# Kernel optimization log

Measured on AMD Instinct MI355X. Metric: run time of the kernel, lower is better.

The kernel has to match this reference:

```python
import jax, jax.numpy as jnp
import numpy as np

LAYERS, HIDDEN, FFN, HEADS = 4, 512, 1024, 4
B, S = 2, 2048
HD = HIDDEN // HEADS  # head size = 128
SCALE_BASE = 512.0
EPS = 1e-5


def _xpos(x, downscale):
    # x: (B, H, S, hd). Faithful to torchscale XPOS with offset=0.
    seq, hd = x.shape[-2], x.shape[-1]
    half = hd // 2
    s = (jnp.arange(0, hd, 2, dtype=jnp.float32) + 0.4 * hd) / (1.4 * hd)  # (half,)
    pos = jnp.arange(seq, dtype=jnp.float32)
    scale = s[None, :] ** (pos[:, None] / SCALE_BASE)  # (S, half)
    inv_freq = 1.0 / (10000.0 ** (jnp.arange(half, dtype=jnp.float32) / half))
    ang = pos[:, None] * inv_freq[None, :]  # (S, half)
    sin, cos = jnp.sin(ang), jnp.cos(ang)
    if downscale:
        scale = 1.0 / scale
    sin_s = jnp.repeat(sin * scale, 2, axis=-1)  # duplicate_interleave -> (S, hd)
    cos_s = jnp.repeat(cos * scale, 2, axis=-1)
    x1, x2 = x[..., ::2], x[..., 1::2]
    rot = jnp.stack([-x2, x1], axis=-1).reshape(x.shape)  # rotate_every_two
    return x * cos_s + rot * sin_s


def _decay_mask(seq, heads):
    gammas = 1.0 - jnp.exp(jnp.linspace(jnp.log(1.0 / 32.0), jnp.log(1.0 / 512.0), heads))
    n = jnp.arange(seq)[:, None]
    m = jnp.arange(seq)[None, :]
    diff = n - m
    pw = gammas[:, None, None] ** jnp.maximum(diff, 0)[None].astype(jnp.float32)
    return jnp.where(diff[None] >= 0, pw, 0.0)  # (H, S, S)


def _ln(x, w, b):
    mu = x.mean(-1, keepdims=True)
    var = x.var(-1, keepdims=True)
    return (x - mu) / jnp.sqrt(var + EPS) * w + b


def _gn(y, w, b, heads):
    # GroupNorm(heads, D) applied on rows of (B*S, D)
    bb, ss, d = y.shape
    hs = d // heads
    yr = y.reshape(bb, ss, heads, hs)
    mu = yr.mean(-1, keepdims=True)
    var = yr.var(-1, keepdims=True)
    yn = ((yr - mu) / jnp.sqrt(var + EPS)).reshape(bb, ss, d)
    return yn * w + b


def setup_inputs() -> dict:
    key = jax.random.key(0)
    ks = jax.random.split(key, 17)
    sc = 1.0 / HIDDEN
    inp = {
        'X': jax.random.normal(ks[0], (B, S, HIDDEN), dtype=jnp.float32),
        'Wq': jax.random.normal(ks[1], (LAYERS, HEADS, HIDDEN, HD), dtype=jnp.float32) * sc,
        'Wk': jax.random.normal(ks[2], (LAYERS, HEADS, HIDDEN, HD), dtype=jnp.float32) * sc,
        'Wv': jax.random.normal(ks[3], (LAYERS, HEADS, HIDDEN, HD), dtype=jnp.float32) * sc,
        'Wg': jax.random.normal(ks[4], (LAYERS, HIDDEN, HIDDEN), dtype=jnp.float32) * sc,
        'Wo': jax.random.normal(ks[5], (LAYERS, HIDDEN, HIDDEN), dtype=jnp.float32) * sc,
        'gn_w': jnp.ones((LAYERS, HIDDEN), dtype=jnp.float32),
        'gn_b': jnp.zeros((LAYERS, HIDDEN), dtype=jnp.float32),
        'ln1_w': jnp.ones((LAYERS, HIDDEN), dtype=jnp.float32),
        'ln1_b': jnp.zeros((LAYERS, HIDDEN), dtype=jnp.float32),
        'ln2_w': jnp.ones((LAYERS, HIDDEN), dtype=jnp.float32),
        'ln2_b': jnp.zeros((LAYERS, HIDDEN), dtype=jnp.float32),
        'f1_w': jax.random.normal(ks[6], (LAYERS, HIDDEN, FFN), dtype=jnp.float32) * (1.0 / np.sqrt(HIDDEN)),
        'f1_b': jnp.zeros((LAYERS, FFN), dtype=jnp.float32),
        'f2_w': jax.random.normal(ks[7], (LAYERS, FFN, HIDDEN), dtype=jnp.float32) * (1.0 / np.sqrt(FFN)),
        'f2_b': jnp.zeros((LAYERS, HIDDEN), dtype=jnp.float32),
    }
    return inp


def reference(X, Wq, Wk, Wv, Wg, Wo, gn_w, gn_b, ln1_w, ln1_b, ln2_w, ln2_b, f1_w, f1_b, f2_w, f2_b):
    bb, ss, d = X.shape
    Dm = _decay_mask(ss, HEADS)  # (H, S, S)
    for i in range(LAYERS):
        Xn = _ln(X, ln1_w[i], ln1_b[i])
        Q = jnp.einsum('bsd,hde->bhse', Xn, Wq[i])
        K = jnp.einsum('bsd,hde->bhse', Xn, Wk[i])
        V = jnp.einsum('bsd,hde->bhse', Xn, Wv[i])
        Q = _xpos(Q, downscale=False)
        K = _xpos(K, downscale=True)
        att = jnp.einsum('bhse,bhte->bhst', Q, K) * Dm[None]
        ret = jnp.einsum('bhst,bhte->bhse', att, V)  # (B,H,S,hd)
        Yh = ret.transpose(0, 2, 1, 3).reshape(bb, ss, d)
        Yg = _gn(Yh, gn_w[i], gn_b[i], HEADS)
        msr = (jax.nn.silu(Xn @ Wg[i]) * Yg) @ Wo[i]
        Y = msr + X
        Yn = _ln(Y, ln2_w[i], ln2_b[i])
        X = jax.nn.gelu(Yn @ f1_w[i] + f1_b[i], approximate=False) @ f2_w[i] + f2_b[i] + Y
    return X
```

## Files before the change

### kernel.cpp

```cpp
#include <hip/hip_runtime.h>
#include <hip/hip_bf16.h>
#include <cstdint>
#include <cstddef>

#define SEQ_ 2048

typedef __bf16 v8bf __attribute__((ext_vector_type(8)));
typedef float v4f __attribute__((ext_vector_type(4)));

__device__ __forceinline__ unsigned short f2bf(float f) {
  unsigned u = __float_as_uint(f);
  return (unsigned short)((u + 0x7FFFu + ((u >> 16) & 1u)) >> 16);
}
__device__ __forceinline__ float bf2f(unsigned short h) {
  return __uint_as_float(((unsigned)h) << 16);
}
__device__ __forceinline__ float silu_(float x) { return x / (1.f + expf(-x)); }
__device__ __forceinline__ float gelu_(float x) { return 0.5f * x * (1.f + erff(x * 0.70710678118654752f)); }

__device__ __forceinline__ void gl_lds16(const void* g, void* l) {
  __builtin_amdgcn_global_load_lds((const __attribute__((address_space(1))) void*)g,
                                   (__attribute__((address_space(3))) void*)l, 16, 0, 0);
}

template <int ROWS>
__device__ __forceinline__ void stage_t(const unsigned short* gsrc, int ldk, char* lds, int tid) {
  const int wid = tid >> 6;
#pragma unroll
  for (int p = 0; p < ROWS / 32; ++p) {
    const int L = p * 256 + tid;
    const int row = L >> 3, slot = L & 7;
    gl_lds16((const char*)(gsrc + (size_t)row * ldk) + ((slot * 16) ^ ((row & 7) << 4)),
             lds + (p * 256 + wid * 64) * 16);
  }
}

__device__ __forceinline__ void stage256(const char* gbase, int srow, char* lds, int tid) {
  const int wid = tid >> 6;
#pragma unroll
  for (int q = 0; q < 8; ++q) {
    const int L = q * 256 + tid;
    const int row = L >> 4;
    const int slot = L & 15;
    gl_lds16(gbase + (size_t)row * srow + ((slot * 16) ^ ((row & 7) << 4)),
             lds + (q * 256 + wid * 64) * 16);
  }
}

__global__ __launch_bounds__(256) void setup_k(const float* __restrict__ Wq, const float* __restrict__ Wk,
                                               const float* __restrict__ Wv, const float* __restrict__ Wg,
                                               const float* __restrict__ Wo, const float* __restrict__ f1w,
                                               const float* __restrict__ f2w, float* __restrict__ tab,
                                               unsigned short* __restrict__ WTQ, unsigned short* __restrict__ WTO,
                                               unsigned short* __restrict__ WF1, unsigned short* __restrict__ WF2) {
  const int b = blockIdx.x, tid = threadIdx.x;
  if (b < 512) {
    const int idx = b * 256 + tid;
    const int pos = idx >> 6, i = idx & 63;
    const float si = (2.f * (float)i + 51.2f) * (1.f / 179.2f);
    const float sc = powf(si, (float)pos * (1.f / 512.f));
    const float invf = powf(10000.f, -(float)i * (1.f / 64.f));
    const float ang = (float)pos * invf;
    const float cs = cosf(ang), sn = sinf(ang);
    tab[idx] = cs * sc;
    tab[131072 + idx] = sn * sc;
    tab[262144 + idx] = cs / sc;
    tab[393216 + idx] = sn / sc;
  } else if (b < 512 + 16384) {
    const size_t idx = (size_t)(b - 512) * 256 + tid;
    const int k = (int)(idx & 511);
    const int n = (int)((idx >> 9) & 2047);
    const int l = (int)(idx >> 20);
    const int sec = n >> 9;
    float v;
    if (sec == 0) {
      const int h = (n >> 7) & 3, e = n & 127;
      v = Wq[(((size_t)l * 4 + h) * 512 + k) * 128 + e];
    } else if (sec == 1) {
      const int h = (n >> 7) & 3, e = n & 127;
      v = Wk[(((size_t)l * 4 + h) * 512 + k) * 128 + e];
    } else if (sec == 2) {
      const int h = (n >> 7) & 3, e = n & 127;
      v = Wv[(((size_t)l * 4 + h) * 512 + k) * 128 + e];
    } else {
      const int c = n & 511;
      v = Wg[((size_t)l * 512 + k) * 512 + c];
    }
    WTQ[idx] = f2bf(v);
  } else if (b < 512 + 16384 + 4096) {
    const size_t idx = (size_t)(b - 512 - 16384) * 256 + tid;
    const int k = (int)(idx & 511);
    const int n = (int)((idx >> 9) & 511);
    const int l = (int)(idx >> 18);
    WTO[idx] = f2bf(Wo[((size_t)l * 512 + k) * 512 + n]);
  } else if (b < 512 + 16384 + 4096 + 8192) {
    const size_t idx = (size_t)(b - 512 - 16384 - 4096) * 256 + tid;
    const int k = (int)(idx & 511);
    const int n = (int)((idx >> 9) & 1023);
    const int l = (int)(idx >> 19);
    WF1[idx] = f2bf(f1w[((size_t)l * 512 + k) * 1024 + n]);
  } else {
    const size_t idx = (size_t)(b - 512 - 16384 - 4096 - 8192) * 256 + tid;
    const int k = (int)(idx & 1023);
    const int n = (int)((idx >> 10) & 511);
    const int l = (int)(idx >> 19);
    WF2[idx] = f2bf(f2w[((size_t)l * 1024 + k) * 512 + n]);
  }
}

__global__ __launch_bounds__(256) void ln_bf_k(const float* __restrict__ x, const float* __restrict__ w,
                                               const float* __restrict__ bv, unsigned short* __restrict__ out) {
  const int row = blockIdx.x * 4 + (threadIdx.x >> 6);
  const int lane = threadIdx.x & 63;
  const float* xr = x + (size_t)row * 512 + lane * 8;
  const float4 v0 = *(const float4*)xr;
  const float4 v1 = *(const float4*)(xr + 4);
  float va[8] = {v0.x, v0.y, v0.z, v0.w, v1.x, v1.y, v1.z, v1.w};
  float s = 0.f, ss = 0.f;
#pragma unroll
  for (int j = 0; j < 8; ++j) { s += va[j]; ss += va[j] * va[j]; }
#pragma unroll
  for (int o = 1; o < 64; o <<= 1) { s += __shfl_xor(s, o); ss += __shfl_xor(ss, o); }
  const float mu = s * (1.f / 512.f);
  const float var = ss * (1.f / 512.f) - mu * mu;
  const float rstd = rsqrtf(var + 1e-5f);
  const int c = lane * 8;
  unsigned short o16[8];
#pragma unroll
  for (int j = 0; j < 8; ++j) o16[j] = f2bf((va[j] - mu) * rstd * w[c + j] + bv[c + j]);
  uint4 pk;
  pk.x = o16[0] | ((unsigned)o16[1] << 16);
  pk.y = o16[2] | ((unsigned)o16[3] << 16);
  pk.z = o16[4] | ((unsigned)o16[5] << 16);
  pk.w = o16[6] | ((unsigned)o16[7] << 16);
  *(uint4*)(out + (size_t)row * 512 + c) = pk;
}

template <int BM, int BN, int EPI>
__global__ __launch_bounds__(256) void mm_k(
    const unsigned short* __restrict__ A, const unsigned short* __restrict__ Bt, const int K,
    const float* __restrict__ t_qc, const float* __restrict__ t_qs,
    const float* __restrict__ t_kc, const float* __restrict__ t_ks,
    unsigned short* __restrict__ o_q, unsigned short* __restrict__ o_k,
    unsigned short* __restrict__ o_ktw, unsigned short* __restrict__ o_vt,
    unsigned short* __restrict__ o_g0,
    const float* __restrict__ auxf, const float* __restrict__ auxf2,
    float* __restrict__ o_f32, unsigned short* __restrict__ o_bf16) {
  constexpr int MR = BM / 32, NR = BN / 32;
  constexpr int BMB = BM * 128, BNB = BN * 128;
  __shared__ __align__(16) char smem[2 * (BMB + BNB)];
  const int tid = threadIdx.x, lane = tid & 63, wid = tid >> 6;
  const int wr = wid >> 1, wc = wid & 1;
  const int l15 = lane & 15, l4 = lane >> 4;
  const int m0 = blockIdx.x * BM, n0 = blockIdx.y * BN;
  const int N = gridDim.y * BN;
  v4f acc[MR][NR];
#pragma unroll
  for (int i = 0; i < MR; ++i)
#pragma unroll
    for (int j = 0; j < NR; ++j) acc[i][j] = v4f{0.f, 0.f, 0.f, 0.f};

  const unsigned short* Ab = A + (size_t)m0 * K;
  const unsigned short* Bb = Bt + (size_t)n0 * K;
  const int NT = K >> 6;
  int cur = 0;
  stage_t<BM>(Ab, K, smem, tid);
  stage_t<BN>(Bb, K, smem + 2 * BMB, tid);
  __syncthreads();
  for (int t = 0; t < NT; ++t) {
    if (t + 1 < NT) {
      stage_t<BM>(Ab + (t + 1) * 64, K, smem + (cur ^ 1) * BMB, tid);
      stage_t<BN>(Bb + (t + 1) * 64, K, smem + 2 * BMB + (cur ^ 1) * BNB, tid);
    }
    const char* Ac = smem + cur * BMB;
    const char* Bc = smem + 2 * BMB + cur * BNB;
#pragma unroll
    for (int ks = 0; ks < 2; ++ks) {
      v8bf af[MR], bfv[NR];
#pragma unroll
      for (int i = 0; i < MR; ++i) {
        const int row = wr * (BM / 2) + i * 16 + l15;
        af[i] = *(const v8bf*)(Ac + row * 128 + ((ks * 64 + l4 * 16) ^ ((row & 7) << 4)));
      }
#pragma unroll
      for (int j = 0; j < NR; ++j) {
        const int row = wc * (BN / 2) + j * 16 + l15;
        bfv[j] = *(const v8bf*)(Bc + row * 128 + ((ks * 64 + l4 * 16) ^ ((row & 7) << 4)));
      }
#pragma unroll
      for (int i = 0; i < MR; ++i)
#pragma unroll
        for (int j = 0; j < NR; ++j)
          acc[i][j] = __builtin_amdgcn_mfma_f32_16x16x32_bf16(af[i], bfv[j], acc[i][j], 0, 0, 0);
    }
    __syncthreads();
    cur ^= 1;
  }

  if constexpr (EPI == 0) {
    const int sec = n0 >> 9;
    const int h = (n0 >> 7) & 3;
    const int srow0 = m0 & (SEQ_ - 1);
    const int bh = ((m0 >> 11) << 2) | h;
    unsigned short* sT = (unsigned short*)smem;
    const float gamma = 1.f - expf(-3.4657359028f - 0.9241962407f * (float)h);
    const float l2g = log2f(gamma);
#pragma unroll
    for (int i = 0; i < MR; ++i) {
#pragma unroll
      for (int r = 0; r < 4; ++r) {
        const int rl = wr * (BM / 2) + i * 16 + l4 * 4 + r;
        const int srow = srow0 + rl;
        const float wk = (sec == 1) ? exp2f(l2g * (float)(127 - (rl & 127))) : 0.f;
#pragma unroll
        for (int j = 0; j < NR; ++j) {
          const int cl = wc * (BN / 2) + j * 16 + l15;
          float v = acc[i][j][r];
          if (sec <= 1) {
            const float p = __shfl_xor(v, 1);
            const float* ct = (sec == 0) ? t_qc : t_kc;
            const float* st = (sec == 0) ? t_qs : t_ks;
            const float c_ = ct[srow * 64 + (cl >> 1)];
            const float s_ = st[srow * 64 + (cl >> 1)];
            const float o = (lane & 1) ? fmaf(v, c_, p * s_) : fmaf(v, c_, -p * s_);
            if (sec == 0) {
              o_q[((size_t)bh * SEQ_ + srow) * 128 + cl] = f2bf(o);
            } else {
              o_k[((size_t)bh * SEQ_ + srow) * 128 + cl] = f2bf(o);
              sT[cl * 136 + rl] = f2bf(o * wk);
            }
          } else if (sec == 2) {
            sT[cl * 136 + rl] = f2bf(v);
          } else {
            o_g0[(size_t)(m0 + rl) * 512 + cl] = f2bf(v);
          }
        }
      }
    }
    if (sec == 1 || sec == 2) {
      __syncthreads();
      unsigned short* dstT = ((sec == 1) ? o_ktw : o_vt) + (size_t)bh * 128 * SEQ_ + srow0;
#pragma unroll
      for (int u = 0; u < 8; ++u) {
        const int idx = u * 256 + tid;
        const int d = idx >> 4, j8 = idx & 15;
        *(v8bf*)(dstT + (size_t)d * SEQ_ + j8 * 8) = *(const v8bf*)(sT + d * 136 + j8 * 8);
      }
    }
  } else {
#pragma unroll
    for (int i = 0; i < MR; ++i) {
#pragma unroll
      for (int r = 0; r < 4; ++r) {
        const int row = m0 + wr * (BM / 2) + i * 16 + l4 * 4 + r;
#pragma unroll
        for (int j = 0; j < NR; ++j) {
          const int col = n0 + wc * (BN / 2) + j * 16 + l15;
          const float v = acc[i][j][r];
          if constexpr (EPI == 1) {
            o_f32[(size_t)row * 512 + col] = v + auxf[(size_t)row * 512 + col];
          } else if constexpr (EPI == 2) {
            o_bf16[(size_t)row * N + col] = f2bf(gelu_(v + auxf[col]));
          } else {
            o_f32[(size_t)row * 512 + col] = v + auxf[col] + auxf2[(size_t)row * 512 + col];
          }
        }
      }
    }
  }
}

__global__ __launch_bounds__(256) void ret1_k(const unsigned short* __restrict__ VT,
                                              const unsigned short* __restrict__ KTw,
                                              float* __restrict__ U) {
  __shared__ __align__(16) char lA[32768];
  __shared__ __align__(16) char lB[32768];
  const int bh = blockIdx.x, c = blockIdx.y;
  const int tid = threadIdx.x, lane = tid & 63, wid = tid >> 6;
  const int wr = wid >> 1, wc = wid & 1;
  const int l15 = lane & 15, l4 = lane >> 4;
  stage256((const char*)(VT + (size_t)bh * 128 * SEQ_ + (size_t)c * 128), SEQ_ * 2, lA, tid);
  stage256((const char*)(KTw + (size_t)bh * 128 * SEQ_ + (size_t)c * 128), SEQ_ * 2, lB, tid);
  __syncthreads();
  v4f acc[4][4];
#pragma unroll
  for (int i = 0; i < 4; ++i)
#pragma unroll
    for (int j = 0; j < 4; ++j) acc[i][j] = v4f{0.f, 0.f, 0.f, 0.f};
#pragma unroll
  for (int ks = 0; ks < 4; ++ks) {
    v8bf af[4], bfv[4];
#pragma unroll
    for (int i = 0; i < 4; ++i) {
      const int ra = wr * 64 + i * 16 + l15;
      af[i] = *(const v8bf*)(lA + ra * 256 + ((ks * 64 + l4 * 16) ^ ((ra & 7) << 4)));
      const int rb = wc * 64 + i * 16 + l15;
      bfv[i] = *(const v8bf*)(lB + rb * 256 + ((ks * 64 + l4 * 16) ^ ((rb & 7) << 4)));
    }
#pragma unroll
    for (int i = 0; i < 4; ++i)
#pragma unroll
      for (int j = 0; j < 4; ++j)
        acc[i][j] = __builtin_amdgcn_mfma_f32_16x16x32_bf16(af[i], bfv[j], acc[i][j], 0, 0, 0);
  }
  float* ub = U + ((size_t)bh * 16 + c) * 16384;
#pragma unroll
  for (int i = 0; i < 4; ++i)
#pragma unroll
    for (int r = 0; r < 4; ++r) {
      const int rd = wr * 64 + i * 16 + l4 * 4 + r;
#pragma unroll
      for (int j = 0; j < 4; ++j) {
        const int ce = wc * 64 + j * 16 + l15;
        ub[rd * 128 + ce] = acc[i][j][r];
      }
    }
}

__global__ __launch_bounds__(256) void ret2_k(const float* __restrict__ U, unsigned short* __restrict__ Sb) {
  const int bh = blockIdx.x;
  const int idx = blockIdx.y * 256 + threadIdx.x;
  const int h = bh & 3;
  const float gamma = 1.f - expf(-3.4657359028f - 0.9241962407f * (float)h);
  const float g128 = exp2f(log2f(gamma) * 128.f);
  float s = 0.f;
#pragma unroll
  for (int c = 0; c < 16; ++c) {
    Sb[((size_t)bh * 16 + c) * 16384 + idx] = f2bf(s);
    s = s * g128 + U[((size_t)bh * 16 + c) * 16384 + idx];
  }
}

__global__ __launch_bounds__(256) void ret3_k(
    const unsigned short* __restrict__ Qb, const unsigned short* __restrict__ Kb,
    const unsigned short* __restrict__ VTb, const unsigned short* __restrict__ Sb,
    const unsigned short* __restrict__ G0b, const float* __restrict__ gnw,
    const float* __restrict__ gnb, unsigned short* __restrict__ Gb) {
  __shared__ __align__(16) char lA[32768];
  __shared__ __align__(16) char lB[32768];
  __shared__ float dpw[132];
  __shared__ float rs[2][128][2];
  const int bh = blockIdx.x, c = blockIdx.y;
  const int h = bh & 3, b = bh >> 2;
  const int tid = threadIdx.x, lane = tid & 63, wid = tid >> 6;
  const int wr = wid >> 1, wc = wid & 1;
  const int l15 = lane & 15, l4 = lane >> 4;
  const float gamma = 1.f - expf(-3.4657359028f - 0.9241962407f * (float)h);
  const float l2g = log2f(gamma);
  stage256((const char*)(Qb + ((size_t)bh * SEQ_ + (size_t)c * 128) * 128), 256, lA, tid);
  stage256((const char*)(Sb + ((size_t)bh * 16 + c) * 16384), 256, lB, tid);
  if (tid < 132) dpw[tid] = exp2f(l2g * (float)tid);
  __syncthreads();

  v4f acc[4][4];
#pragma unroll
  for (int i = 0; i < 4; ++i)
#pragma unroll
    for (int j = 0; j < 4; ++j) acc[i][j] = v4f{0.f, 0.f, 0.f, 0.f};

#pragma unroll
  for (int ks = 0; ks < 4; ++ks) {
    v8bf af[4], bfv[4];
#pragma unroll
    for (int i = 0; i < 4; ++i) {
      const int ra = wr * 64 + i * 16 + l15;
      af[i] = *(const v8bf*)(lA + ra * 256 + ((ks * 64 + l4 * 16) ^ ((ra & 7) << 4)));
      const int rb = wc * 64 + i * 16 + l15;
      bfv[i] = *(const v8bf*)(lB + rb * 256 + ((ks * 64 + l4 * 16) ^ ((rb & 7) << 4)));
    }
#pragma unroll
    for (int i = 0; i < 4; ++i)
#pragma unroll
      for (int j = 0; j < 4; ++j)
        acc[i][j] = __builtin_amdgcn_mfma_f32_16x16x32_bf16(af[i], bfv[j], acc[i][j], 0, 0, 0);
  }
#pragma unroll
  for (int i = 0; i < 4; ++i)
#pragma unroll
    for (int r = 0; r < 4; ++r) {
      const float sc = dpw[wr * 64 + i * 16 + l4 * 4 + r + 1];
#pragma unroll
      for (int j = 0; j < 4; ++j) acc[i][j][r] *= sc;
    }
  __syncthreads();
  stage256((const char*)(Kb + ((size_t)bh * SEQ_ + (size_t)c * 128) * 128), 256, lB, tid);
  __syncthreads();

  v4f sacc[4][4];
#pragma unroll
  for (int i = 0; i < 4; ++i)
#pragma unroll
    for (int j = 0; j < 4; ++j) sacc[i][j] = v4f{0.f, 0.f, 0.f, 0.f};
#pragma unroll
  for (int ks = 0; ks < 4; ++ks) {
    v8bf af[4], bfv[4];
#pragma unroll
    for (int i = 0; i < 4; ++i) {
      const int ra = wr * 64 + i * 16 + l15;
      af[i] = *(const v8bf*)(lA + ra * 256 + ((ks * 64 + l4 * 16) ^ ((ra & 7) << 4)));
      const int rb = wc * 64 + i * 16 + l15;
      bfv[i] = *(const v8bf*)(lB + rb * 256 + ((ks * 64 + l4 * 16) ^ ((rb & 7) << 4)));
    }
#pragma unroll
    for (int i = 0; i < 4; ++i)
#pragma unroll
      for (int j = 0; j < 4; ++j)
        sacc[i][j] = __builtin_amdgcn_mfma_f32_16x16x32_bf16(af[i], bfv[j], sacc[i][j], 0, 0, 0);
  }
  __syncthreads();

#pragma unroll
  for (int i = 0; i < 4; ++i)
#pragma unroll
    for (int r = 0; r < 4; ++r) {
      const int jrow = wr * 64 + i * 16 + l4 * 4 + r;
#pragma unroll
      for (int j = 0; j < 4; ++j) {
        const int icol = wc * 64 + j * 16 + l15;
        const int d = jrow - icol;
        const int dc = d < 0 ? 0 : d;
        const float wgt = dpw[dc];
        const float p = (d < 0) ? 0.f : sacc[i][j][r] * wgt;
        *(unsigned short*)(lB + jrow * 256 + ((icol * 2) ^ ((jrow & 7) << 4))) = f2bf(p);
      }
    }
  stage256((const char*)(VTb + (size_t)bh * 128 * SEQ_ + (size_t)c * 128), SEQ_ * 2, lA, tid);
  __syncthreads();

#pragma unroll
  for (int ks = 0; ks < 4; ++ks) {
    v8bf af[4], bfv[4];
#pragma unroll
    for (int i = 0; i < 4; ++i) {
      const int ra = wr * 64 + i * 16 + l15;
      af[i] = *(const v8bf*)(lB + ra * 256 + ((ks * 64 + l4 * 16) ^ ((ra & 7) << 4)));
      const int rb = wc * 64 + i * 16 + l15;
      bfv[i] = *(const v8bf*)(lA + rb * 256 + ((ks * 64 + l4 * 16) ^ ((rb & 7) << 4)));
    }
#pragma unroll
    for (int i = 0; i < 4; ++i)
#pragma unroll
      for (int j = 0; j < 4; ++j)
        acc[i][j] = __builtin_amdgcn_mfma_f32_16x16x32_bf16(af[i], bfv[j], acc[i][j], 0, 0, 0);
  }

#pragma unroll
  for (int i = 0; i < 4; ++i)
#pragma unroll
    for (int r = 0; r < 4; ++r) {
      const int jrow = wr * 64 + i * 16 + l4 * 4 + r;
      float s1 = 0.f, s2 = 0.f;
#pragma unroll
      for (int j = 0; j < 4; ++j) { const float v = acc[i][j][r]; s1 += v; s2 += v * v; }
#pragma unroll
      for (int o = 1; o < 16; o <<= 1) { s1 += __shfl_xor(s1, o); s2 += __shfl_xor(s2, o); }
      if (l15 == 0) { rs[wc][jrow][0] = s1; rs[wc][jrow][1] = s2; }
    }
  __syncthreads();
  const int tbase = b * SEQ_ + c * 128;
#pragma unroll
  for (int i = 0; i < 4; ++i)
#pragma unroll
    for (int r = 0; r < 4; ++r) {
      const int jrow = wr * 64 + i * 16 + l4 * 4 + r;
      const float s1 = rs[0][jrow][0] + rs[1][jrow][0];
      const float s2 = rs[0][jrow][1] + rs[1][jrow][1];
      const float mu = s1 * (1.f / 128.f);
      const float var = s2 * (1.f / 128.f) - mu * mu;
      const float rstd = rsqrtf(var + 1e-5f);
      const size_t t = (size_t)(tbase + jrow);
#pragma unroll
      for (int j = 0; j < 4; ++j) {
        const int dd = wc * 64 + j * 16 + l15;
        const int cc = h * 128 + dd;
        const float g0 = bf2f(G0b[t * 512 + cc]);
        float o = (acc[i][j][r] - mu) * rstd * gnw[cc] + gnb[cc];
        o *= silu_(g0);
        Gb[t * 512 + cc] = f2bf(o);
      }
    }
}

extern "C" void kernel_launch(void* const* d_in, const int* in_sizes, int n_in,
                              void* d_out, int out_size, void* d_ws, size_t ws_size,
                              hipStream_t stream) {
  const float* X = (const float*)d_in[0];
  const float* Wq = (const float*)d_in[1];
  const float* Wk = (const float*)d_in[2];
  const float* Wv = (const float*)d_in[3];
  const float* Wg = (const float*)d_in[4];
  const float* Wo = (const float*)d_in[5];
  const float* gnw = (const float*)d_in[6];
  const float* gnb = (const float*)d_in[7];
  const float* ln1w = (const float*)d_in[8];
  const float* ln1b = (const float*)d_in[9];
  const float* ln2w = (const float*)d_in[10];
  const float* ln2b = (const float*)d_in[11];
  const float* f1w = (const float*)d_in[12];
  const float* f1b = (const float*)d_in[13];
  const float* f2w = (const float*)d_in[14];
  const float* f2b = (const float*)d_in[15];

  char* ws = (char*)d_ws;
  float* TAB = (float*)(ws + 0);
  unsigned short* WTQ = (unsigned short*)(ws + 2097152);
  unsigned short* WTO = (unsigned short*)(ws + 10485760);
  unsigned short* WF1 = (unsigned short*)(ws + 12582912);
  unsigned short* WF2 = (unsigned short*)(ws + 16777216);
  unsigned short* XNb = (unsigned short*)(ws + 20971520);
  unsigned short* Qb  = (unsigned short*)(ws + 25165824);
  unsigned short* Kb  = (unsigned short*)(ws + 29360128);
  unsigned short* KTw = (unsigned short*)(ws + 33554432);
  unsigned short* VTb = (unsigned short*)(ws + 37748736);
  unsigned short* G0b = (unsigned short*)(ws + 46137344);
  unsigned short* Sbf = (unsigned short*)(ws + 50331648);
  unsigned short* Gb  = (unsigned short*)(ws + 54525952);
  float* Y   = (float*)(ws + 58720256);
  float* XB  = (float*)(ws + 67108864);
  unsigned short* F1b = (unsigned short*)(ws + 75497472);
  float* U = (float*)(ws + 75497472);
  float* qc = TAB, * qs = TAB + 131072, * kc = TAB + 262144, * ks = TAB + 393216;

  setup_k<<<37376, 256, 0, stream>>>(Wq, Wk, Wv, Wg, Wo, f1w, f2w, TAB, WTQ, WTO, WF1, WF2);

  const float* Xcur = X;
  for (int l = 0; l < 4; ++l) {
    ln_bf_k<<<1024, 256, 0, stream>>>(Xcur, ln1w + l * 512, ln1b + l * 512, XNb);
    mm_k<128, 128, 0><<<dim3(32, 16), 256, 0, stream>>>(
        XNb, WTQ + (size_t)l * 2048 * 512, 512, qc, qs, kc, ks,
        Qb, Kb, KTw, VTb, G0b, nullptr, nullptr, nullptr, nullptr);
    ret1_k<<<dim3(8, 16), 256, 0, stream>>>(VTb, KTw, U);
    ret2_k<<<dim3(8, 64), 256, 0, stream>>>(U, Sbf);
    ret3_k<<<dim3(8, 16), 256, 0, stream>>>(Qb, Kb, VTb, Sbf, G0b,
                                            gnw + l * 512, gnb + l * 512, Gb);
    mm_k<128, 64, 1><<<dim3(32, 8), 256, 0, stream>>>(
        Gb, WTO + (size_t)l * 512 * 512, 512, nullptr, nullptr, nullptr, nullptr,
        nullptr, nullptr, nullptr, nullptr, nullptr, Xcur, nullptr, Y, nullptr);
    ln_bf_k<<<1024, 256, 0, stream>>>(Y, ln2w + l * 512, ln2b + l * 512, XNb);
    mm_k<128, 128, 2><<<dim3(32, 8), 256, 0, stream>>>(
        XNb, WF1 + (size_t)l * 1024 * 512, 512, nullptr, nullptr, nullptr, nullptr,
        nullptr, nullptr, nullptr, nullptr, nullptr, f1b + l * 1024, nullptr, nullptr, F1b);
    float* outX = (l == 3) ? (float*)d_out : XB;
    mm_k<128, 64, 3><<<dim3(32, 8), 256, 0, stream>>>(
        F1b, WF2 + (size_t)l * 512 * 1024, 1024, nullptr, nullptr, nullptr, nullptr,
        nullptr, nullptr, nullptr, nullptr, nullptr, f2b + l * 512, Y, outX, nullptr);
    Xcur = XB;
  }
}
```

Baseline: 572.7 us.

## Split retention chunk kernel into half-chunks and tile weight transpose via LDS

The retention kernel ret3_k now handles half a 128-row chunk per block, doubling the grid from 128 to 256 blocks. The first half skips the causally-masked upper part of the intra-chunk QK^T and PV products, which cuts wasted MFMA work and raises occupancy on a GPU with many CUs. Separately, the setup kernel transposes and converts the weights in 64x64 tiles through shared memory with vectorized loads and stores, replacing a strided per-element gather. The cost is more code and duplicated Q/S staging across the two half blocks.

```diff
diff --git a/kernel.cpp b/kernel.cpp
--- a/kernel.cpp
+++ b/kernel.cpp
@@ -35,10 +35,11 @@
   }
 }
 
-__device__ __forceinline__ void stage256(const char* gbase, int srow, char* lds, int tid) {
+template <int NROWS>
+__device__ __forceinline__ void stage_rows(const char* gbase, int srow, char* lds, int tid) {
   const int wid = tid >> 6;
 #pragma unroll
-  for (int q = 0; q < 8; ++q) {
+  for (int q = 0; q < NROWS / 16; ++q) {
     const int L = q * 256 + tid;
     const int row = L >> 4;
     const int slot = L & 15;
@@ -66,45 +67,71 @@
     tab[131072 + idx] = sn * sc;
     tab[262144 + idx] = cs / sc;
     tab[393216 + idx] = sn / sc;
-  } else if (b < 512 + 16384) {
-    const size_t idx = (size_t)(b - 512) * 256 + tid;
-    const int k = (int)(idx & 511);
-    const int n = (int)((idx >> 9) & 2047);
-    const int l = (int)(idx >> 20);
-    const int sec = n >> 9;
-    float v;
-    if (sec == 0) {
-      const int h = (n >> 7) & 3, e = n & 127;
-      v = Wq[(((size_t)l * 4 + h) * 512 + k) * 128 + e];
-    } else if (sec == 1) {
-      const int h = (n >> 7) & 3, e = n & 127;
-      v = Wk[(((size_t)l * 4 + h) * 512 + k) * 128 + e];
-    } else if (sec == 2) {
-      const int h = (n >> 7) & 3, e = n & 127;
-      v = Wv[(((size_t)l * 4 + h) * 512 + k) * 128 + e];
-    } else {
-      const int c = n & 511;
-      v = Wg[((size_t)l * 512 + k) * 512 + c];
-    }
-    WTQ[idx] = f2bf(v);
-  } else if (b < 512 + 16384 + 4096) {
-    const size_t idx = (size_t)(b - 512 - 16384) * 256 + tid;
-    const int k = (int)(idx & 511);
-    const int n = (int)((idx >> 9) & 511);
-    const int l = (int)(idx >> 18);
-    WTO[idx] = f2bf(Wo[((size_t)l * 512 + k) * 512 + n]);
-  } else if (b < 512 + 16384 + 4096 + 8192) {
-    const size_t idx = (size_t)(b - 512 - 16384 - 4096) * 256 + tid;
-    const int k = (int)(idx & 511);
-    const int n = (int)((idx >> 9) & 1023);
-    const int l = (int)(idx >> 19);
-    WF1[idx] = f2bf(f1w[((size_t)l * 512 + k) * 1024 + n]);
+    return;
+  }
+  __shared__ float t[64][65];
+  const float* src;
+  unsigned short* dst;
+  int ldn, ldk;
+  int b2 = b - 512;
+  if (b2 < 768) {
+    const int l = b2 / 192, r = b2 % 192, sec = r / 64, r2 = r % 64, h = r2 >> 4, tt = r2 & 15;
+    const int kt = tt >> 1, et = tt & 1;
+    const float* W = (sec == 0) ? Wq : (sec == 1) ? Wk : Wv;
+    src = W + (((size_t)(l * 4 + h) * 512 + kt * 64) * 128 + et * 64);
+    ldn = 128;
+    dst = WTQ + (size_t)l * 1048576 + (size_t)(sec * 512 + h * 128 + et * 64) * 512 + kt * 64;
+    ldk = 512;
+  } else if (b2 < 1024) {
+    b2 -= 768;
+    const int l = b2 >> 6, tt = b2 & 63, kt = tt >> 3, nt = tt & 7;
+    src = Wg + (size_t)l * 262144 + (size_t)kt * 64 * 512 + nt * 64;
+    ldn = 512;
+    dst = WTQ + (size_t)l * 1048576 + (size_t)(1536 + nt * 64) * 512 + kt * 64;
+    ldk = 512;
+  } else if (b2 < 1280) {
+    b2 -= 1024;
+    const int l = b2 >> 6, tt = b2 & 63, kt = tt >> 3, nt = tt & 7;
+    src = Wo + (size_t)l * 262144 + (size_t)kt * 64 * 512 + nt * 64;
+    ldn = 512;
+    dst = WTO + (size_t)l * 262144 + (size_t)nt * 64 * 512 + kt * 64;
+    ldk = 512;
+  } else if (b2 < 1792) {
+    b2 -= 1280;
+    const int l = b2 >> 7, tt = b2 & 127, kt = tt >> 4, nt = tt & 15;
+    src = f1w + (size_t)l * 524288 + (size_t)kt * 64 * 1024 + nt * 64;
+    ldn = 1024;
+    dst = WF1 + (size_t)l * 524288 + (size_t)nt * 64 * 512 + kt * 64;
+    ldk = 512;
   } else {
-    const size_t idx = (size_t)(b - 512 - 16384 - 4096 - 8192) * 256 + tid;
-    const int k = (int)(idx & 1023);
-    const int n = (int)((idx >> 10) & 511);
-    const int l = (int)(idx >> 19);
-    WF2[idx] = f2bf(f2w[((size_t)l * 1024 + k) * 512 + n]);
+    b2 -= 1792;
+    const int l = b2 >> 7, tt = b2 & 127, kt = tt >> 3, nt = tt & 7;
+    src = f2w + (size_t)l * 524288 + (size_t)kt * 64 * 512 + nt * 64;
+    ldn = 512;
+    dst = WF2 + (size_t)l * 524288 + (size_t)nt * 64 * 1024 + kt * 64;
+    ldk = 1024;
+  }
+#pragma unroll
+  for (int p = 0; p < 4; ++p) {
+    const int idx = p * 256 + tid;
+    const int kr = idx >> 4, c4 = (idx & 15) * 4;
+    const float4 v = *(const float4*)(src + (size_t)kr * ldn + c4);
+    t[kr][c4] = v.x; t[kr][c4 + 1] = v.y; t[kr][c4 + 2] = v.z; t[kr][c4 + 3] = v.w;
+  }
+  __syncthreads();
+#pragma unroll
+  for (int p = 0; p < 2; ++p) {
+    const int idx = p * 256 + tid;
+    const int nr = idx >> 3, k8 = (idx & 7) * 8;
+    unsigned short o[8];
+#pragma unroll
+    for (int j = 0; j < 8; ++j) o[j] = f2bf(t[k8 + j][nr]);
+    uint4 pk;
+    pk.x = o[0] | ((unsigned)o[1] << 16);
+    pk.y = o[2] | ((unsigned)o[3] << 16);
+    pk.z = o[4] | ((unsigned)o[5] << 16);
+    pk.w = o[6] | ((unsigned)o[7] << 16);
+    *(uint4*)(dst + (size_t)nr * ldk + k8) = pk;
   }
 }
 
@@ -279,8 +306,8 @@
   const int tid = threadIdx.x, lane = tid & 63, wid = tid >> 6;
   const int wr = wid >> 1, wc = wid & 1;
   const int l15 = lane & 15, l4 = lane >> 4;
-  stage256((const char*)(VT + (size_t)bh * 128 * SEQ_ + (size_t)c * 128), SEQ_ * 2, lA, tid);
-  stage256((const char*)(KTw + (size_t)bh * 128 * SEQ_ + (size_t)c * 128), SEQ_ * 2, lB, tid);
+  stage_rows<128>((const char*)(VT + (size_t)bh * 128 * SEQ_ + (size_t)c * 128), SEQ_ * 2, lA, tid);
+  stage_rows<128>((const char*)(KTw + (size_t)bh * 128 * SEQ_ + (size_t)c * 128), SEQ_ * 2, lB, tid);
   __syncthreads();
   v4f acc[4][4];
 #pragma unroll
@@ -331,144 +358,155 @@
   }
 }
 
-__global__ __launch_bounds__(256) void ret3_k(
-    const unsigned short* __restrict__ Qb, const unsigned short* __restrict__ Kb,
-    const unsigned short* __restrict__ VTb, const unsigned short* __restrict__ Sb,
-    const unsigned short* __restrict__ G0b, const float* __restrict__ gnw,
-    const float* __restrict__ gnb, unsigned short* __restrict__ Gb) {
-  __shared__ __align__(16) char lA[32768];
-  __shared__ __align__(16) char lB[32768];
-  __shared__ float dpw[132];
-  __shared__ float rs[2][128][2];
-  const int bh = blockIdx.x, c = blockIdx.y;
+template <int HF>
+__device__ __forceinline__ void ret3_body(
+    const unsigned short* Qb, const unsigned short* Kb, const unsigned short* VTb,
+    const unsigned short* Sb, const unsigned short* G0b, const float* gnw,
+    const float* gnb, unsigned short* Gb, char* lA, char* lB, const float* dpw,
+    float* rs, int bh, int c, int tid) {
   const int h = bh & 3, b = bh >> 2;
-  const int tid = threadIdx.x, lane = tid & 63, wid = tid >> 6;
+  const int lane = tid & 63, wid = tid >> 6;
   const int wr = wid >> 1, wc = wid & 1;
   const int l15 = lane & 15, l4 = lane >> 4;
-  const float gamma = 1.f - expf(-3.4657359028f - 0.9241962407f * (float)h);
-  const float l2g = log2f(gamma);
-  stage256((const char*)(Qb + ((size_t)bh * SEQ_ + (size_t)c * 128) * 128), 256, lA, tid);
-  stage256((const char*)(Sb + ((size_t)bh * 16 + c) * 16384), 256, lB, tid);
-  if (tid < 132) dpw[tid] = exp2f(l2g * (float)tid);
-  __syncthreads();
-
-  v4f acc[4][4];
-#pragma unroll
-  for (int i = 0; i < 4; ++i)
+  constexpr int NS = 2 + 2 * HF;
+  constexpr int KS = 2 + 2 * HF;
+  const int j0 = c * 128 + HF * 64;
+
+  stage_rows<64>((const char*)(Qb + ((size_t)bh * SEQ_ + j0) * 128), 256, lA, tid);
+  stage_rows<128>((const char*)(Sb + ((size_t)bh * 16 + c) * 16384), 256, lB, tid);
+  __syncthreads();
+
+  v4f acc[2][4];
+#pragma unroll
+  for (int i = 0; i < 2; ++i)
 #pragma unroll
     for (int j = 0; j < 4; ++j) acc[i][j] = v4f{0.f, 0.f, 0.f, 0.f};
-
 #pragma unroll
   for (int ks = 0; ks < 4; ++ks) {
-    v8bf af[4], bfv[4];
-#pragma unroll
-    for (int i = 0; i < 4; ++i) {
-      const int ra = wr * 64 + i * 16 + l15;
+    v8bf af[2], bfv[4];
+#pragma unroll
+    for (int i = 0; i < 2; ++i) {
+      const int ra = wr * 32 + i * 16 + l15;
       af[i] = *(const v8bf*)(lA + ra * 256 + ((ks * 64 + l4 * 16) ^ ((ra & 7) << 4)));
-      const int rb = wc * 64 + i * 16 + l15;
-      bfv[i] = *(const v8bf*)(lB + rb * 256 + ((ks * 64 + l4 * 16) ^ ((rb & 7) << 4)));
-    }
-#pragma unroll
-    for (int i = 0; i < 4; ++i)
+    }
+#pragma unroll
+    for (int j = 0; j < 4; ++j) {
+      const int rb = wc * 64 + j * 16 + l15;
+      bfv[j] = *(const v8bf*)(lB + rb * 256 + ((ks * 64 + l4 * 16) ^ ((rb & 7) << 4)));
+    }
+#pragma unroll
+    for (int i = 0; i < 2; ++i)
 #pragma unroll
       for (int j = 0; j < 4; ++j)
         acc[i][j] = __builtin_amdgcn_mfma_f32_16x16x32_bf16(af[i], bfv[j], acc[i][j], 0, 0, 0);
   }
 #pragma unroll
-  for (int i = 0; i < 4; ++i)
+  for (int i = 0; i < 2; ++i)
 #pragma unroll
     for (int r = 0; r < 4; ++r) {
-      const float sc = dpw[wr * 64 + i * 16 + l4 * 4 + r + 1];
+      const float sc = dpw[HF * 64 + wr * 32 + i * 16 + l4 * 4 + r + 1];
 #pragma unroll
       for (int j = 0; j < 4; ++j) acc[i][j][r] *= sc;
     }
   __syncthreads();
-  stage256((const char*)(Kb + ((size_t)bh * SEQ_ + (size_t)c * 128) * 128), 256, lB, tid);
-  __syncthreads();
-
-  v4f sacc[4][4];
-#pragma unroll
-  for (int i = 0; i < 4; ++i)
-#pragma unroll
-    for (int j = 0; j < 4; ++j) sacc[i][j] = v4f{0.f, 0.f, 0.f, 0.f};
+  if constexpr (HF == 0)
+    stage_rows<64>((const char*)(Kb + ((size_t)bh * SEQ_ + c * 128) * 128), 256, lB, tid);
+  else
+    stage_rows<128>((const char*)(Kb + ((size_t)bh * SEQ_ + c * 128) * 128), 256, lB, tid);
+  __syncthreads();
+
+  v4f sacc[2][NS];
+#pragma unroll
+  for (int i = 0; i < 2; ++i)
+#pragma unroll
+    for (int j = 0; j < NS; ++j) sacc[i][j] = v4f{0.f, 0.f, 0.f, 0.f};
 #pragma unroll
   for (int ks = 0; ks < 4; ++ks) {
-    v8bf af[4], bfv[4];
-#pragma unroll
-    for (int i = 0; i < 4; ++i) {
-      const int ra = wr * 64 + i * 16 + l15;
+    v8bf af[2], bfv[NS];
+#pragma unroll
+    for (int i = 0; i < 2; ++i) {
+      const int ra = wr * 32 + i * 16 + l15;
       af[i] = *(const v8bf*)(lA + ra * 256 + ((ks * 64 + l4 * 16) ^ ((ra & 7) << 4)));
-      const int rb = wc * 64 + i * 16 + l15;
-      bfv[i] = *(const v8bf*)(lB + rb * 256 + ((ks * 64 + l4 * 16) ^ ((rb & 7) << 4)));
-    }
-#pragma unroll
-    for (int i = 0; i < 4; ++i)
-#pragma unroll
-      for (int j = 0; j < 4; ++j)
+    }
+#pragma unroll
+    for (int j = 0; j < NS; ++j) {
+      const int rb = wc * (16 * NS) + j * 16 + l15;
+      bfv[j] = *(const v8bf*)(lB + rb * 256 + ((ks * 64 + l4 * 16) ^ ((rb & 7) << 4)));
+    }
+#pragma unroll
+    for (int i = 0; i < 2; ++i)
+#pragma unroll
+      for (int j = 0; j < NS; ++j)
         sacc[i][j] = __builtin_amdgcn_mfma_f32_16x16x32_bf16(af[i], bfv[j], sacc[i][j], 0, 0, 0);
   }
   __syncthreads();
 
 #pragma unroll
-  for (int i = 0; i < 4; ++i)
+  for (int i = 0; i < 2; ++i)
 #pragma unroll
     for (int r = 0; r < 4; ++r) {
-      const int jrow = wr * 64 + i * 16 + l4 * 4 + r;
-#pragma unroll
-      for (int j = 0; j < 4; ++j) {
-        const int icol = wc * 64 + j * 16 + l15;
-        const int d = jrow - icol;
-        const int dc = d < 0 ? 0 : d;
-        const float wgt = dpw[dc];
-        const float p = (d < 0) ? 0.f : sacc[i][j][r] * wgt;
-        *(unsigned short*)(lB + jrow * 256 + ((icol * 2) ^ ((jrow & 7) << 4))) = f2bf(p);
-      }
-    }
-  stage256((const char*)(VTb + (size_t)bh * 128 * SEQ_ + (size_t)c * 128), SEQ_ * 2, lA, tid);
-  __syncthreads();
-
-#pragma unroll
-  for (int ks = 0; ks < 4; ++ks) {
-    v8bf af[4], bfv[4];
-#pragma unroll
-    for (int i = 0; i < 4; ++i) {
-      const int ra = wr * 64 + i * 16 + l15;
-      af[i] = *(const v8bf*)(lB + ra * 256 + ((ks * 64 + l4 * 16) ^ ((ra & 7) << 4)));
-      const int rb = wc * 64 + i * 16 + l15;
-      bfv[i] = *(const v8bf*)(lA + rb * 256 + ((ks * 64 + l4 * 16) ^ ((rb & 7) << 4)));
-    }
-#pragma unroll
-    for (int i = 0; i < 4; ++i)
+      const int jl = wr * 32 + i * 16 + l4 * 4 + r;
+#pragma unroll
+      for (int j = 0; j < NS; ++j) {
+        const int icol = wc * (16 * NS) + j * 16 + l15;
+        const int d = HF * 64 + jl - icol;
+        const float p = (d < 0) ? 0.f : sacc[i][j][r] * dpw[d];
+        *(unsigned short*)(lA + jl * 256 + ((icol * 2) ^ ((jl & 7) << 4))) = f2bf(p);
+      }
+    }
+  if constexpr (HF == 0)
+    stage_t<128>(VTb + (size_t)bh * 128 * SEQ_ + (size_t)c * 128, SEQ_, lB, tid);
+  else
+    stage_rows<128>((const char*)(VTb + (size_t)bh * 128 * SEQ_ + (size_t)c * 128), SEQ_ * 2, lB, tid);
+  __syncthreads();
+
+#pragma unroll
+  for (int ks = 0; ks < KS; ++ks) {
+    v8bf af[2], bfv[4];
+#pragma unroll
+    for (int i = 0; i < 2; ++i) {
+      const int ra = wr * 32 + i * 16 + l15;
+      af[i] = *(const v8bf*)(lA + ra * 256 + ((ks * 64 + l4 * 16) ^ ((ra & 7) << 4)));
+    }
+#pragma unroll
+    for (int j = 0; j < 4; ++j) {
+      const int rb = wc * 64 + j * 16 + l15;
+      if constexpr (HF == 0)
+        bfv[j] = *(const v8bf*)(lB + rb * 128 + ((ks * 64 + l4 * 16) ^ ((rb & 7) << 4)));
+      else
+        bfv[j] = *(const v8bf*)(lB + rb * 256 + ((ks * 64 + l4 * 16) ^ ((rb & 7) << 4)));
+    }
+#pragma unroll
+    for (int i = 0; i < 2; ++i)
 #pragma unroll
       for (int j = 0; j < 4; ++j)
         acc[i][j] = __builtin_amdgcn_mfma_f32_16x16x32_bf16(af[i], bfv[j], acc[i][j], 0, 0, 0);
   }
 
 #pragma unroll
-  for (int i = 0; i < 4; ++i)
+  for (int i = 0; i < 2; ++i)
 #pragma unroll
     for (int r = 0; r < 4; ++r) {
-      const int jrow = wr * 64 + i * 16 + l4 * 4 + r;
+      const int jl = wr * 32 + i * 16 + l4 * 4 + r;
       float s1 = 0.f, s2 = 0.f;
 #pragma unroll
       for (int j = 0; j < 4; ++j) { const float v = acc[i][j][r]; s1 += v; s2 += v * v; }
 #pragma unroll
       for (int o = 1; o < 16; o <<= 1) { s1 += __shfl_xor(s1, o); s2 += __shfl_xor(s2, o); }
-      if (l15 == 0) { rs[wc][jrow][0] = s1; rs[wc][jrow][1] = s2; }
-    }
-  __syncthreads();
-  const int tbase = b * SEQ_ + c * 128;
-#pragma unroll
-  for (int i = 0; i < 4; ++i)
+      if (l15 == 0) { rs[(wc * 64 + jl) * 2] = s1; rs[(wc * 64 + jl) * 2 + 1] = s2; }
+    }
+  __syncthreads();
+#pragma unroll
+  for (int i = 0; i < 2; ++i)
 #pragma unroll
     for (int r = 0; r < 4; ++r) {
-      const int jrow = wr * 64 + i * 16 + l4 * 4 + r;
-      const float s1 = rs[0][jrow][0] + rs[1][jrow][0];
-      const float s2 = rs[0][jrow][1] + rs[1][jrow][1];
+      const int jl = wr * 32 + i * 16 + l4 * 4 + r;
+      const float s1 = rs[jl * 2] + rs[(64 + jl) * 2];
+      const float s2 = rs[jl * 2 + 1] + rs[(64 + jl) * 2 + 1];
       const float mu = s1 * (1.f / 128.f);
       const float var = s2 * (1.f / 128.f) - mu * mu;
       const float rstd = rsqrtf(var + 1e-5f);
-      const size_t t = (size_t)(tbase + jrow);
+      const size_t t = (size_t)(b * SEQ_ + j0 + jl);
 #pragma unroll
       for (int j = 0; j < 4; ++j) {
         const int dd = wc * 64 + j * 16 + l15;
@@ -479,6 +517,28 @@
         Gb[t * 512 + cc] = f2bf(o);
       }
     }
+}
+
+__global__ __launch_bounds__(256) void ret3_k(
+    const unsigned short* __restrict__ Qb, const unsigned short* __restrict__ Kb,
+    const unsigned short* __restrict__ VTb, const unsigned short* __restrict__ Sb,
+    const unsigned short* __restrict__ G0b, const float* __restrict__ gnw,
+    const float* __restrict__ gnb, unsigned short* __restrict__ Gb) {
+  __shared__ __align__(16) char lA[16384];
+  __shared__ __align__(16) char lB[32768];
+  __shared__ float dpw[132];
+  __shared__ float rs[128 * 2];
+  const int bh = blockIdx.x;
+  const int hf = blockIdx.y & 1, c = blockIdx.y >> 1;
+  const int tid = threadIdx.x;
+  const int h = bh & 3;
+  const float gamma = 1.f - expf(-3.4657359028f - 0.9241962407f * (float)h);
+  const float l2g = log2f(gamma);
+  if (tid < 132) dpw[tid] = exp2f(l2g * (float)tid);
+  if (hf == 0)
+    ret3_body<0>(Qb, Kb, VTb, Sb, G0b, gnw, gnb, Gb, lA, lB, dpw, rs, bh, c, tid);
+  else
+    ret3_body<1>(Qb, Kb, VTb, Sb, G0b, gnw, gnb, Gb, lA, lB, dpw, rs, bh, c, tid);
 }
 
 extern "C" void kernel_launch(void* const* d_in, const int* in_sizes, int n_in,
@@ -521,7 +581,7 @@
   float* U = (float*)(ws + 75497472);
   float* qc = TAB, * qs = TAB + 131072, * kc = TAB + 262144, * ks = TAB + 393216;
 
-  setup_k<<<37376, 256, 0, stream>>>(Wq, Wk, Wv, Wg, Wo, f1w, f2w, TAB, WTQ, WTO, WF1, WF2);
+  setup_k<<<2816, 256, 0, stream>>>(Wq, Wk, Wv, Wg, Wo, f1w, f2w, TAB, WTQ, WTO, WF1, WF2);
 
   const float* Xcur = X;
   for (int l = 0; l < 4; ++l) {
@@ -531,7 +591,7 @@
         Qb, Kb, KTw, VTb, G0b, nullptr, nullptr, nullptr, nullptr);
     ret1_k<<<dim3(8, 16), 256, 0, stream>>>(VTb, KTw, U);
     ret2_k<<<dim3(8, 64), 256, 0, stream>>>(U, Sbf);
-    ret3_k<<<dim3(8, 16), 256, 0, stream>>>(Qb, Kb, VTb, Sbf, G0b,
+    ret3_k<<<dim3(8, 32), 256, 0, stream>>>(Qb, Kb, VTb, Sbf, G0b,
                                             gnw + l * 512, gnb + l * 512, Gb);
     mm_k<128, 64, 1><<<dim3(32, 8), 256, 0, stream>>>(
         Gb, WTO + (size_t)l * 512 * 512, 512, nullptr, nullptr, nullptr, nullptr,
```

Measured after the change: 505.2 us (median of 2 runs). 1.13x faster.
